# Kernel tuning notes

Hardware: AMD Instinct MI355X
Metric: run time of the kernel (lower is better)

Reference implementation:

```python
import jax, jax.numpy as jnp
import numpy as np
from jax import lax

N_NODES = 100000
N_EDGES = 3200000
NODE_DIM = 128
K = 8            # number of kmeans heads
MAX_OVERLAP = 2  # top-k cluster memberships per node
THRESH = 1e-8


def setup_inputs() -> dict:
    key = jax.random.key(0)
    k1, k2, k3, k4, k5 = jax.random.split(key, 5)
    x = jax.random.normal(k1, (N_NODES, NODE_DIM), dtype=jnp.float32)
    edge_index = jax.random.randint(k2, (2, N_EDGES), 0, N_NODES, dtype=jnp.int64)
    # binary initial cluster-membership masks [N, K] (float, like KMeansCarry.mask)
    mask = (jax.random.uniform(k3, (N_NODES, K)) > 0.5).astype(jnp.float32)
    Ww = jax.random.normal(k4, (K, NODE_DIM, NODE_DIM), dtype=jnp.float32) * (1.0 / np.sqrt(NODE_DIM))
    Wm = jax.random.normal(k5, (K, NODE_DIM, 1), dtype=jnp.float32) * (1.0 / np.sqrt(NODE_DIM))
    return {"x": x, "edge_index": edge_index, "mask": mask, "Ww": Ww, "Wm": Wm}


def reference(x, edge_index, mask, Ww, Wm):
    """KMeans over graph: k heads -> boolean node scores -> norm-weighted top-k assignment."""
    N = x.shape[0]
    src, dst = edge_index[0], edge_index[1]

    def head(m_col, Ww_i, Wm_i):
        # masked node features (KMeansCarry.masked_x)
        xm = x * m_col[:, None]                                   # [N, D]
        node_mask = m_col > 0                                     # [N]
        # masked subgraph (KMeansCarry.masked_edge_index): keep edges with both endpoints in mask
        ev = (node_mask[src] & node_mask[dst]).astype(x.dtype)    # [E]
        # weighting module: per-node transform
        w = jax.nn.relu(xm @ Ww_i)                                # [N, D]
        # message passing over masked subgraph (irregular gather/scatter)
        agg = jax.ops.segment_sum(w[src] * ev[:, None], dst, num_segments=N)  # [N, D]
        # mask module score -> act -> threshold at 0 (KMeansHead.forward)
        score = ((xm + agg) @ Wm_i)[:, 0]                         # [N]
        return jnp.tanh(score) > 0                                # bool [N]

    # vmap over the K heads
    head_masks = jax.vmap(head, in_axes=(1, 0, 0), out_axes=1)(mask, Ww, Wm)  # [N, K] bool

    # KMeans.forward combine step
    above_thresh = head_masks  # bool > THRESH (1e-8 < 1) == the bool itself
    norms = jnp.linalg.norm(x, axis=1, keepdims=True)             # [N, 1]
    masked_weights = jnp.where(above_thresh, norms, -jnp.inf)     # [N, K]
    top_vals, top_idx = lax.top_k(masked_weights, MAX_OVERLAP)    # [N, MAX_OVERLAP]
    valid = jnp.isfinite(top_vals)
    # scatter ones at (row, top_idx) where valid  (duplicate-safe via one-hot + min)
    oh = jax.nn.one_hot(top_idx, K, dtype=x.dtype) * valid[..., None].astype(x.dtype)
    final_mask = jnp.minimum(oh.sum(axis=1), 1.0)                 # [N, K]
    return final_mask
```

## Files before the change

kernel.cpp:

```cpp
#include <hip/hip_runtime.h>

#define N_NODES 100000
#define N_EDGES 3200000
#define D 128
#define K 8

#define TAU 4e-3f
#define WL_CAP 262144

#define CHUNK 96
#define GWAVES 8

#define BKT 128
#define NB  ((N_NODES + BKT - 1) / BKT)
#define EPB 16384
#define NEB ((N_EDGES + EPB - 1) / EPB)

typedef float  f32x4  __attribute__((ext_vector_type(4)));
typedef __bf16 bf16x8 __attribute__((ext_vector_type(8)));

static __device__ __forceinline__ unsigned short bfbits(float f)
{
    const __bf16 b = (__bf16)f;
    return __builtin_bit_cast(unsigned short, b);
}
static __device__ __forceinline__ float bfback(unsigned short u)
{
    return (float)__builtin_bit_cast(__bf16, u);
}

#define NCOMPACT ((N_NODES + 255) / 256)
#define NWSPLIT  ((K * D * D + 255) / 256)

__global__ __launch_bounds__(256)
void prep_kernel(const float* __restrict__ mask,
                 int* __restrict__ lists,
                 int* __restrict__ cnts,
                 unsigned char* __restrict__ mb,
                 const float* __restrict__ Ww,
                 unsigned short* __restrict__ wtH,
                 unsigned short* __restrict__ wtL)
{
    __shared__ int wcnt[4][K];
    __shared__ int wbase[4][K];

    if (blockIdx.x >= NCOMPACT) {
        const int t = (blockIdx.x - NCOMPACT) * 256 + threadIdx.x;
        if (t >= K * D * D) return;
        const int k   = t >> 14;
        const int kk  = (t >> 7) & 127;
        const int col = t & 127;
        const float v = Ww[t];
        const __bf16 h = (__bf16)v;
        const __bf16 l = (__bf16)(v - (float)h);
        const int o = (k << 14) | (col << 7) | kk;
        wtH[o] = __builtin_bit_cast(unsigned short, h);
        wtL[o] = __builtin_bit_cast(unsigned short, l);
        return;
    }

    const int n = blockIdx.x * 256 + threadIdx.x;
    const int lane = threadIdx.x & 63;
    const int wave = threadIdx.x >> 6;
    const bool valid = (n < N_NODES);

    unsigned long long ball[K];
    int bits8 = 0;
    #pragma unroll
    for (int k = 0; k < K; ++k) {
        const bool m = valid && (mask[(size_t)n * K + k] > 0.0f);
        bits8 |= m ? (1 << k) : 0;
        ball[k] = __ballot(m);
        if (lane == 0) wcnt[wave][k] = __popcll(ball[k]);
    }
    __syncthreads();

    if (threadIdx.x < K) {
        const int k = threadIdx.x;
        const int t0 = wcnt[0][k], t1 = wcnt[1][k], t2 = wcnt[2][k], t3 = wcnt[3][k];
        const int base = (t0 + t1 + t2 + t3)
                       ? atomicAdd(&cnts[k], t0 + t1 + t2 + t3) : 0;
        wbase[0][k] = base;
        wbase[1][k] = base + t0;
        wbase[2][k] = base + t0 + t1;
        wbase[3][k] = base + t0 + t1 + t2;
    }
    __syncthreads();

    #pragma unroll
    for (int k = 0; k < K; ++k) {
        if ((ball[k] >> lane) & 1ull) {
            const int pos = __popcll(ball[k] & ((1ull << lane) - 1ull));
            lists[(size_t)k * N_NODES + wbase[wave][k] + pos] = n;
        }
    }
    if (valid) mb[n] = (unsigned char)bits8;
}

__global__ __launch_bounds__(512, 4)
void head_gemm_kernel(const float* __restrict__ x,
                      const unsigned short* __restrict__ wtH,
                      const unsigned short* __restrict__ wtL,
                      const float* __restrict__ Wm,
                      const int* __restrict__ lists,
                      const int* __restrict__ cnts,
                      float* __restrict__ t32,
                      float* __restrict__ base32,
                      const int* __restrict__ ei,
                      int* __restrict__ bhist,
                      const int nhg)
{
    __shared__ __align__(16) unsigned short Ah[CHUNK * D];
    __shared__ __align__(16) unsigned short Al[CHUNK * D];
    __shared__ float redT[GWAVES][48];
    __shared__ float redB[CHUNK][4];
    __shared__ int   ids[CHUNK];

    const int tid = threadIdx.x;

    if (blockIdx.x >= nhg) {
        int* lh = (int*)Ah;
        for (int i = tid; i < NB; i += 512) lh[i] = 0;
        __syncthreads();
        const int e0 = (blockIdx.x - nhg) * EPB;
        #pragma unroll 4
        for (int i = 0; i < EPB / 512; ++i) {
            const int e = e0 + i * 512 + tid;
            if (e < N_EDGES) atomicAdd(&lh[ei[(long long)N_EDGES + e] >> 7], 1);
        }
        __syncthreads();
        for (int i = tid; i < NB; i += 512) {
            const int c = lh[i];
            if (c) atomicAdd(&bhist[i], c);
        }
        return;
    }

    const int bid = blockIdx.x;
    const int k = (bid >> 3) & 7;
    const int c = ((bid >> 6) << 3) | (bid & 7);

    const int cnt = cnts[k];
    const int nbase = c * CHUNK;
    if (nbase >= cnt) return;

    const int lane = tid & 63;
    const int wave = __builtin_amdgcn_readfirstlane((int)(tid >> 6));
    const int* list = lists + (size_t)k * N_NODES;

    if (tid < CHUNK) {
        int idx = nbase + tid;
        if (idx >= cnt) idx = cnt - 1;
        ids[tid] = list[idx];
    }
    __syncthreads();

    if (tid < CHUNK * 4) {
        const int r = tid >> 2;
        const int q = tid & 3;
        const int id = ids[r];
        const float4* xr  = (const float4*)(x + (size_t)id * D);
        const float4* wm4 = (const float4*)(Wm + k * D);
        float bp = 0.0f;
        #pragma unroll
        for (int i = 0; i < 8; ++i) {
            const int f4 = q + 4 * i;
            const float4 v  = xr[f4];
            const float4 wv = wm4[f4];
            bp += v.x * wv.x + v.y * wv.y + v.z * wv.z + v.w * wv.w;
            ushort4 h, l;
            h.x = bfbits(v.x); l.x = bfbits(v.x - bfback(h.x));
            h.y = bfbits(v.y); l.y = bfbits(v.y - bfback(h.y));
            h.z = bfbits(v.z); l.z = bfbits(v.z - bfback(h.z));
            h.w = bfbits(v.w); l.w = bfbits(v.w - bfback(h.w));
            const int boff = ((r * 256 + f4 * 8) ^ ((r & 7) << 4)) >> 1;
            *(ushort4*)&Ah[boff] = h;
            *(ushort4*)&Al[boff] = l;
        }
        redB[r][q] = bp;
    }
    __syncthreads();

    const int wm_ = wave >> 2;
    const int wn  = wave & 3;
    const int l15 = lane & 15;
    const int lg  = lane >> 4;
    const int n0  = wn * 32;

    f32x4 acc[3][2];
    #pragma unroll
    for (int mf = 0; mf < 3; ++mf) {
        acc[mf][0] = (f32x4){0.f, 0.f, 0.f, 0.f};
        acc[mf][1] = (f32x4){0.f, 0.f, 0.f, 0.f};
    }

    const unsigned short* bH0 = wtH + (((k * D + n0 + l15) << 7) + 8 * lg);
    const unsigned short* bH1 = bH0 + (16 << 7);
    const unsigned short* bL0 = wtL + (((k * D + n0 + l15) << 7) + 8 * lg);
    const unsigned short* bL1 = bL0 + (16 << 7);

    #pragma unroll
    for (int s = 0; s < 4; ++s) {
        const int ko = s * 32;
        const bf16x8 Bh0 = *reinterpret_cast<const bf16x8*>(bH0 + ko);
        const bf16x8 Bh1 = *reinterpret_cast<const bf16x8*>(bH1 + ko);
        const bf16x8 Bl0 = *reinterpret_cast<const bf16x8*>(bL0 + ko);
        const bf16x8 Bl1 = *reinterpret_cast<const bf16x8*>(bL1 + ko);
        #pragma unroll
        for (int mf = 0; mf < 3; ++mf) {
            const int m = wm_ * 48 + mf * 16 + l15;
            const int byt = (m * 256 + (ko + 8 * lg) * 2) ^ ((m & 7) << 4);
            const bf16x8 Amh = *reinterpret_cast<const bf16x8*>(&Ah[byt >> 1]);
            const bf16x8 Aml = *reinterpret_cast<const bf16x8*>(&Al[byt >> 1]);
            acc[mf][0] = __builtin_amdgcn_mfma_f32_16x16x32_bf16(Amh, Bh0, acc[mf][0], 0, 0, 0);
            acc[mf][1] = __builtin_amdgcn_mfma_f32_16x16x32_bf16(Amh, Bh1, acc[mf][1], 0, 0, 0);
            acc[mf][0] = __builtin_amdgcn_mfma_f32_16x16x32_bf16(Amh, Bl0, acc[mf][0], 0, 0, 0);
            acc[mf][1] = __builtin_amdgcn_mfma_f32_16x16x32_bf16(Amh, Bl1, acc[mf][1], 0, 0, 0);
            acc[mf][0] = __builtin_amdgcn_mfma_f32_16x16x32_bf16(Aml, Bh0, acc[mf][0], 0, 0, 0);
            acc[mf][1] = __builtin_amdgcn_mfma_f32_16x16x32_bf16(Aml, Bh1, acc[mf][1], 0, 0, 0);
        }
    }

    const float wmv0 = Wm[k * D + n0 + l15];
    const float wmv1 = Wm[k * D + n0 + 16 + l15];
    float keep = 0.0f;
    #pragma unroll
    for (int mf = 0; mf < 3; ++mf) {
        #pragma unroll
        for (int r = 0; r < 4; ++r) {
            float p = fmaxf(acc[mf][0][r], 0.0f) * wmv0
                    + fmaxf(acc[mf][1][r], 0.0f) * wmv1;
            p += __shfl_xor(p, 1);
            p += __shfl_xor(p, 2);
            p += __shfl_xor(p, 4);
            p += __shfl_xor(p, 8);
            if (l15 == mf * 4 + r) keep = p;
        }
    }
    if (l15 < 12)
        redT[wave][((l15 >> 2) << 4) + (lg << 2) + (l15 & 3)] = keep;
    __syncthreads();

    if (tid < CHUNK) {
        const int r = tid;
        const int idx = nbase + r;
        if (idx < cnt) {
            const int wg = r / 48;
            const int rl = r - wg * 48;
            const float ts = redT[wg * 4 + 0][rl] + redT[wg * 4 + 1][rl]
                           + redT[wg * 4 + 2][rl] + redT[wg * 4 + 3][rl];
            const float bs = redB[r][0] + redB[r][1] + redB[r][2] + redB[r][3];
            const int id = ids[r];
            t32[(size_t)id * K + k]    = ts;
            base32[(size_t)id * K + k] = bs;
        }
    }
}

__global__ __launch_bounds__(1024)
void escan_kernel(const int* __restrict__ bhist,
                  int* __restrict__ bases,
                  int* __restrict__ cursors)
{
    __shared__ int sc[1024];
    const int tid = threadIdx.x;
    const int v = (tid < NB) ? bhist[tid] : 0;
    sc[tid] = v;
    __syncthreads();
    for (int off = 1; off < 1024; off <<= 1) {
        int t = 0;
        if (tid >= off) t = sc[tid - off];
        __syncthreads();
        sc[tid] += t;
        __syncthreads();
    }
    if (tid < NB) {
        const int ex = sc[tid] - v;
        bases[tid]   = ex;
        cursors[tid] = ex;
        if (tid == NB - 1) bases[NB] = sc[tid];
    }
}

__global__ __launch_bounds__(512)
void ebucket_kernel(const int* __restrict__ ei,
                    int* __restrict__ cursors,
                    int* __restrict__ bkt)
{
    __shared__ int lh[NB];
    __shared__ int wb[NB];
    const int tid = threadIdx.x;
    for (int i = tid; i < NB; i += 512) lh[i] = 0;
    __syncthreads();
    const int e0 = blockIdx.x * EPB;
    #pragma unroll 4
    for (int i = 0; i < EPB / 512; ++i) {
        const int e = e0 + i * 512 + tid;
        if (e < N_EDGES) atomicAdd(&lh[ei[(long long)N_EDGES + e] >> 7], 1);
    }
    __syncthreads();
    for (int i = tid; i < NB; i += 512) {
        const int c = lh[i];
        wb[i] = c ? atomicAdd(&cursors[i], c) : 0;
        lh[i] = 0;
    }
    __syncthreads();
    #pragma unroll 4
    for (int i = 0; i < EPB / 512; ++i) {
        const int e = e0 + i * 512 + tid;
        if (e < N_EDGES) {
            const int d = ei[(long long)N_EDGES + e];
            const int s = ei[e];
            const int b = d >> 7;
            const int r = atomicAdd(&lh[b], 1);
            const int idx = wb[b] + r;
            if (idx < N_EDGES)
                bkt[idx] = (s << 7) | (d & 127);
        }
    }
}

__global__ __launch_bounds__(512)
void eaccum_kernel(const int* __restrict__ bkt,
                   const int* __restrict__ bases,
                   const unsigned char* __restrict__ mb,
                   const float* __restrict__ t32,
                   const float* __restrict__ base32,
                   float* __restrict__ agg32,
                   float* __restrict__ out,
                   unsigned char* __restrict__ flag8,
                   double* __restrict__ s64,
                   int2* __restrict__ wl,
                   int* __restrict__ wlcnt)
{
    __shared__ float acc[BKT * K];
    __shared__ unsigned char mbl[BKT];
    __shared__ unsigned char fll[BKT];
    __shared__ int anyfl;
    const int b = blockIdx.x;
    const int n0 = b << 7;
    const int tid = threadIdx.x;
    for (int i = tid; i < BKT * K; i += 512) acc[i] = 0.0f;
    if (tid < BKT) {
        const int n = n0 + tid;
        mbl[tid] = (n < N_NODES) ? mb[n] : 0;
    }
    if (tid == 0) anyfl = 0;
    __syncthreads();

    const int eB = bases[b];
    int eE = bases[b + 1];
    if (eE > N_EDGES) eE = N_EDGES;
    for (int e = eB + tid; e < eE; e += 512) {
        const int rec = bkt[e];
        const int s  = rec >> 7;
        const int dl = rec & 127;
        const unsigned md = mbl[dl];
        if (md) {
            const float4* tr = (const float4*)(t32 + (size_t)s * K);
            const float4 t0 = tr[0], t1 = tr[1];
            #pragma unroll
            for (int k = 0; k < K; ++k) {
                const float tv = (k < 4)
                    ? ((k < 2) ? (k == 0 ? t0.x : t0.y) : (k == 2 ? t0.z : t0.w))
                    : ((k < 6) ? (k == 4 ? t1.x : t1.y) : (k == 6 ? t1.z : t1.w));
                if (((md >> k) & 1) && tv != 0.0f)
                    atomicAdd(&acc[(dl << 3) + k], tv);
            }
        }
    }
    __syncthreads();

    if (tid < BKT) {
        const int n = n0 + tid;
        if (n < N_NODES) {
            const unsigned m8 = mbl[tid];
            const float4* b4 = (const float4*)(base32 + (size_t)n * K);
            const float4 b40 = b4[0], b41 = b4[1];
            float bs[K];
            bs[0] = b40.x; bs[1] = b40.y; bs[2] = b40.z; bs[3] = b40.w;
            bs[4] = b41.x; bs[5] = b41.y; bs[6] = b41.z; bs[7] = b41.w;
            float o[K];
            int cnt = 0, fl = 0;
            #pragma unroll
            for (int k = 0; k < K; ++k) {
                const float sc = bs[k] + acc[(tid << 3) + k];
                const bool masked = (m8 >> k) & 1;
                const bool hm = masked && (sc > 0.0f);
                if (masked && fabsf(sc) < TAU) fl |= (1 << k);
                o[k] = (hm && cnt < 2) ? 1.0f : 0.0f;
                cnt += hm ? 1 : 0;
            }
            float4* op = (float4*)(out + (size_t)n * K);
            op[0] = make_float4(o[0], o[1], o[2], o[3]);
            op[1] = make_float4(o[4], o[5], o[6], o[7]);
            float4* ap = (float4*)(agg32 + (size_t)n * K);
            ap[0] = make_float4(acc[(tid << 3) + 0], acc[(tid << 3) + 1],
                                acc[(tid << 3) + 2], acc[(tid << 3) + 3]);
            ap[1] = make_float4(acc[(tid << 3) + 4], acc[(tid << 3) + 5],
                                acc[(tid << 3) + 6], acc[(tid << 3) + 7]);
            flag8[n] = (unsigned char)fl;
            fll[tid] = (unsigned char)fl;
            if (fl) {
                anyfl = 1;
                #pragma unroll
                for (int k = 0; k < K; ++k)
                    if ((fl >> k) & 1) s64[(size_t)n * K + k] = 0.0;
            }
        } else {
            fll[tid] = 0;
        }
    }
    __syncthreads();

    if (anyfl) {
        for (int e = eB + tid; e < eE; e += 512) {
            const int rec = bkt[e];
            const int dl = rec & 127;
            unsigned f = fll[dl];
            if (!f) continue;
            const int s = rec >> 7;
            f &= mb[s];
            while (f) {
                const int k = __ffs(f) - 1;
                f &= f - 1;
                const int idx = atomicAdd(wlcnt, 1);
                if (idx < WL_CAP) wl[idx] = make_int2(s | (k << 20), n0 + dl);
            }
        }
    }
}

__global__ __launch_bounds__(256)
void scatter_fallback_kernel(const int* __restrict__ ei,
                             const unsigned char* __restrict__ mb,
                             const float* __restrict__ t32,
                             float* __restrict__ agg32)
{
    const long long tid = (long long)blockIdx.x * 256 + threadIdx.x;
    if (tid >= (long long)N_EDGES * K) return;
    const int k = (int)(tid & (K - 1));
    const long long e = tid >> 3;
    const int d = ei[(long long)N_EDGES + e];
    const int s = ei[e];
    const unsigned md = mb[d] & mb[s];
    if (!((md >> k) & 1)) return;
    const float v = t32[(size_t)s * K + k];
    if (v != 0.0f) atomicAdd(&agg32[(size_t)d * K + k], v);
}

__global__ __launch_bounds__(256)
void combine_flag_kernel(const unsigned char* __restrict__ mb,
                         const float* __restrict__ base32,
                         const float* __restrict__ agg32,
                         float* __restrict__ out,
                         unsigned char* __restrict__ flag8,
                         double* __restrict__ s64)
{
    const int n = blockIdx.x * 256 + threadIdx.x;
    if (n >= N_NODES) return;
    const unsigned m8 = mb[n];
    float o[K];
    int cnt = 0, fl = 0;
    #pragma unroll
    for (int k = 0; k < K; ++k) {
        const float s = base32[(size_t)n * K + k] + agg32[(size_t)n * K + k];
        const bool masked = (m8 >> k) & 1;
        const bool hm = masked && (s > 0.0f);
        if (masked && fabsf(s) < TAU) fl |= (1 << k);
        o[k] = (hm && cnt < 2) ? 1.0f : 0.0f;
        cnt += hm ? 1 : 0;
    }
    float4* op = (float4*)(out + (size_t)n * K);
    op[0] = make_float4(o[0], o[1], o[2], o[3]);
    op[1] = make_float4(o[4], o[5], o[6], o[7]);
    flag8[n] = (unsigned char)fl;
    if (fl) {
        #pragma unroll
        for (int k = 0; k < K; ++k)
            if ((fl >> k) & 1) s64[(size_t)n * K + k] = 0.0;
    }
}

__global__ __launch_bounds__(256)
void edge_flag_kernel(const int* __restrict__ ei,
                      const unsigned char* __restrict__ mb,
                      const unsigned char* __restrict__ flag8,
                      int2* __restrict__ wl,
                      int* __restrict__ wlcnt)
{
    const int e = blockIdx.x * 256 + threadIdx.x;
    if (e >= N_EDGES) return;
    const int d = ei[(long long)N_EDGES + e];
    unsigned f = flag8[d];
    if (!f) return;
    const int s = ei[e];
    f &= mb[s];
    while (f) {
        const int k = __ffs(f) - 1;
        f &= f - 1;
        const int idx = atomicAdd(wlcnt, 1);
        if (idx < WL_CAP) wl[idx] = make_int2(s | (k << 20), d);
    }
}

__global__ __launch_bounds__(256)
void repair_t_kernel(const float* __restrict__ x,
                     const float* __restrict__ Ww,
                     const float* __restrict__ Wm,
                     const int2* __restrict__ wl,
                     const int* __restrict__ wlcnt,
                     double* __restrict__ score64)
{
    const int lane = threadIdx.x & 63;
    const int waveId = blockIdx.x * 4 + (threadIdx.x >> 6);
    const int nWaves = gridDim.x * 4;
    int cnt = *wlcnt;
    if (cnt > WL_CAP) cnt = WL_CAP;
    for (int w = waveId; w < cnt; w += nWaves) {
        const int2 ent = wl[w];
        const int s = __builtin_amdgcn_readfirstlane(ent.x & 0xFFFFF);
        const int k = __builtin_amdgcn_readfirstlane(ent.x >> 20);
        const int d = ent.y;
        const float* xr = x + (size_t)s * D;
        const float* Wk = Ww + (size_t)k * D * D;
        double c0 = 0.0, c1 = 0.0;
        for (int j = 0; j < D; ++j) {
            const double xd = (double)xr[j];
            c0 = fma(xd, (double)Wk[j * D + lane], c0);
            c1 = fma(xd, (double)Wk[j * D + lane + 64], c1);
        }
        double ts = fmax(c0, 0.0) * (double)Wm[k * D + lane]
                  + fmax(c1, 0.0) * (double)Wm[k * D + lane + 64];
        #pragma unroll
        for (int off = 32; off > 0; off >>= 1) ts += __shfl_xor(ts, off);
        if (lane == 0) atomicAdd(&score64[(size_t)d * K + k], ts);
    }
}

__global__ __launch_bounds__(256)
void repair_combine_kernel(const float* __restrict__ x,
                           const unsigned char* __restrict__ mb,
                           const float* __restrict__ Wm,
                           const float* __restrict__ base32,
                           const float* __restrict__ agg32,
                           const double* __restrict__ score64,
                           const unsigned char* __restrict__ flag8,
                           float* __restrict__ out)
{
    const int n = blockIdx.x * 256 + threadIdx.x;
    if (n >= N_NODES) return;
    const unsigned f = flag8[n];
    if (!f) return;
    const unsigned m8 = mb[n];
    float o[K];
    int cnt = 0;
    #pragma unroll
    for (int k = 0; k < K; ++k) {
        bool hm;
        if ((f >> k) & 1) {
            double b = 0.0;
            for (int j = 0; j < D; ++j)
                b = fma((double)x[(size_t)n * D + j], (double)Wm[k * D + j], b);
            hm = (b + score64[(size_t)n * K + k]) > 0.0;
        } else {
            hm = ((m8 >> k) & 1) &&
                 ((base32[(size_t)n * K + k] + agg32[(size_t)n * K + k]) > 0.0f);
        }
        o[k] = (hm && cnt < 2) ? 1.0f : 0.0f;
        cnt += hm ? 1 : 0;
    }
    float4* op = (float4*)(out + (size_t)n * K);
    op[0] = make_float4(o[0], o[1], o[2], o[3]);
    op[1] = make_float4(o[4], o[5], o[6], o[7]);
}

extern "C" void kernel_launch(void* const* d_in, const int* in_sizes, int n_in,
                              void* d_out, int out_size, void* d_ws, size_t ws_size,
                              hipStream_t stream)
{
    const float* x    = (const float*)d_in[0];
    const int*   ei   = (const int*)d_in[1];
    const float* mask = (const float*)d_in[2];
    const float* Ww   = (const float*)d_in[3];
    const float* Wm   = (const float*)d_in[4];
    float* out = (float*)d_out;

    char* w = (char*)d_ws;
    float*          t32    = (float*)w;
    float*          agg32  = (float*)(w + 3200000);
    double*         s64    = (double*)(w + 6400000);
    int*            lists  = (int*)(w + 6400000);
    unsigned short* wtH    = (unsigned short*)(w + 9600000);
    unsigned short* wtL    = (unsigned short*)(w + 9600000 + 262144);
    unsigned char*  flag8  = (unsigned char*)(w + 12800000);
    int*            cnts   = (int*)(w + 12900000);
    int*            wlcnt  = (int*)(w + 12900032);
    int*            bhist  = (int*)(w + 12900064);
    int*            bases  = (int*)(w + 12903200);
    int*            cursors= (int*)(w + 12906336);
    int2*           wl     = (int2*)(w + 12909504);
    float*          b32    = (float*)(w + 15006656);
    unsigned char*  mb     = (unsigned char*)(w + 18206656);
    int*            bkt    = (int*)(w + 18306656);
    const size_t WS_BUCKETED = 31106656;
    const bool bucketed = (ws_size >= WS_BUCKETED);

    hipMemsetAsync(t32, 0, 3200000, stream);
    hipMemsetAsync(w + 12900000, 0, 4096, stream);

    prep_kernel<<<NCOMPACT + NWSPLIT, 256, 0, stream>>>(
        mask, lists, cnts, mb, Ww, wtH, wtL);

    const int nchunks = (N_NODES + CHUNK - 1) / CHUNK;
    const int nc8 = (nchunks + 7) & ~7;
    const int nhg = nc8 * K;
    head_gemm_kernel<<<nhg + NEB, 512, 0, stream>>>(
        x, wtH, wtL, Wm, lists, cnts, t32, b32, ei, bhist, nhg);

    if (bucketed) {
        escan_kernel<<<1, 1024, 0, stream>>>(bhist, bases, cursors);
        ebucket_kernel<<<NEB, 512, 0, stream>>>(ei, cursors, bkt);
        eaccum_kernel<<<NB, 512, 0, stream>>>(bkt, bases, mb, t32, b32,
                                              agg32, out, flag8, s64, wl, wlcnt);
    } else {
        hipMemsetAsync(agg32, 0, 3200000, stream);
        const long long nek = (long long)N_EDGES * K;
        scatter_fallback_kernel<<<(int)((nek + 255) / 256), 256, 0, stream>>>(
            ei, mb, t32, agg32);
        combine_flag_kernel<<<(N_NODES + 255) / 256, 256, 0, stream>>>(
            mb, b32, agg32, out, flag8, s64);
        edge_flag_kernel<<<(N_EDGES + 255) / 256, 256, 0, stream>>>(
            ei, mb, flag8, wl, wlcnt);
    }

    repair_t_kernel<<<512, 256, 0, stream>>>(x, Ww, Wm, wl, wlcnt, s64);

    repair_combine_kernel<<<(N_NODES + 255) / 256, 256, 0, stream>>>(
        x, mb, Wm, b32, agg32, s64, flag8, out);
}
```

Measured before the change: 359.1 us.

## Move edge histogram into prep kernel and overlap bucketing with head GEMM

The destination-bucket histogram moves from the GEMM kernel into extra blocks of the prep kernel, and the prefix scan now runs before the head GEMM. The edge-bucketing scatter then runs as leading blocks of the head GEMM launch, which removes the separate ebucket kernel launch and overlaps the memory-bound bucketing with compute-bound GEMM blocks. In exchange the prep kernel gets heavier, and the bucketing blocks share occupancy with the GEMM blocks.

```diff
diff --git a/kernel.cpp b/kernel.cpp
--- a/kernel.cpp
+++ b/kernel.cpp
@@ -39,10 +39,30 @@
                  unsigned char* __restrict__ mb,
                  const float* __restrict__ Ww,
                  unsigned short* __restrict__ wtH,
-                 unsigned short* __restrict__ wtL)
-{
-    __shared__ int wcnt[4][K];
-    __shared__ int wbase[4][K];
+                 unsigned short* __restrict__ wtL,
+                 const int* __restrict__ ei,
+                 int* __restrict__ bhist)
+{
+    __shared__ int lds[NB + 64];
+
+    if (blockIdx.x >= NCOMPACT + NWSPLIT) {
+        int* lh = lds;
+        const int tid = threadIdx.x;
+        for (int i = tid; i < NB; i += 256) lh[i] = 0;
+        __syncthreads();
+        const int e0 = (blockIdx.x - NCOMPACT - NWSPLIT) * EPB;
+        #pragma unroll 4
+        for (int i = 0; i < EPB / 256; ++i) {
+            const int e = e0 + i * 256 + tid;
+            if (e < N_EDGES) atomicAdd(&lh[ei[(long long)N_EDGES + e] >> 7], 1);
+        }
+        __syncthreads();
+        for (int i = tid; i < NB; i += 256) {
+            const int c = lh[i];
+            if (c) atomicAdd(&bhist[i], c);
+        }
+        return;
+    }
 
     if (blockIdx.x >= NCOMPACT) {
         const int t = (blockIdx.x - NCOMPACT) * 256 + threadIdx.x;
@@ -59,6 +79,9 @@
         return;
     }
 
+    int (*wcnt)[K]  = (int(*)[K])lds;
+    int (*wbase)[K] = (int(*)[K])(lds + 32);
+
     const int n = blockIdx.x * 256 + threadIdx.x;
     const int lane = threadIdx.x & 63;
     const int wave = threadIdx.x >> 6;
@@ -107,8 +130,9 @@
                       float* __restrict__ t32,
                       float* __restrict__ base32,
                       const int* __restrict__ ei,
-                      int* __restrict__ bhist,
-                      const int nhg)
+                      int* __restrict__ cursors,
+                      int* __restrict__ bkt,
+                      const int neb)
 {
     __shared__ __align__(16) unsigned short Ah[CHUNK * D];
     __shared__ __align__(16) unsigned short Al[CHUNK * D];
@@ -118,11 +142,12 @@
 
     const int tid = threadIdx.x;
 
-    if (blockIdx.x >= nhg) {
+    if ((int)blockIdx.x < neb) {
         int* lh = (int*)Ah;
+        int* wb = lh + NB;
         for (int i = tid; i < NB; i += 512) lh[i] = 0;
         __syncthreads();
-        const int e0 = (blockIdx.x - nhg) * EPB;
+        const int e0 = blockIdx.x * EPB;
         #pragma unroll 4
         for (int i = 0; i < EPB / 512; ++i) {
             const int e = e0 + i * 512 + tid;
@@ -131,12 +156,27 @@
         __syncthreads();
         for (int i = tid; i < NB; i += 512) {
             const int c = lh[i];
-            if (c) atomicAdd(&bhist[i], c);
+            wb[i] = c ? atomicAdd(&cursors[i], c) : 0;
+            lh[i] = 0;
+        }
+        __syncthreads();
+        #pragma unroll 4
+        for (int i = 0; i < EPB / 512; ++i) {
+            const int e = e0 + i * 512 + tid;
+            if (e < N_EDGES) {
+                const int d = ei[(long long)N_EDGES + e];
+                const int s = ei[e];
+                const int b = d >> 7;
+                const int r = atomicAdd(&lh[b], 1);
+                const int idx = wb[b] + r;
+                if (idx < N_EDGES)
+                    bkt[idx] = (s << 7) | (d & 127);
+            }
         }
         return;
     }
 
-    const int bid = blockIdx.x;
+    const int bid = blockIdx.x - neb;
     const int k = (bid >> 3) & 7;
     const int c = ((bid >> 6) << 3) | (bid & 7);
 
@@ -279,44 +319,6 @@
         bases[tid]   = ex;
         cursors[tid] = ex;
         if (tid == NB - 1) bases[NB] = sc[tid];
-    }
-}
-
-__global__ __launch_bounds__(512)
-void ebucket_kernel(const int* __restrict__ ei,
-                    int* __restrict__ cursors,
-                    int* __restrict__ bkt)
-{
-    __shared__ int lh[NB];
-    __shared__ int wb[NB];
-    const int tid = threadIdx.x;
-    for (int i = tid; i < NB; i += 512) lh[i] = 0;
-    __syncthreads();
-    const int e0 = blockIdx.x * EPB;
-    #pragma unroll 4
-    for (int i = 0; i < EPB / 512; ++i) {
-        const int e = e0 + i * 512 + tid;
-        if (e < N_EDGES) atomicAdd(&lh[ei[(long long)N_EDGES + e] >> 7], 1);
-    }
-    __syncthreads();
-    for (int i = tid; i < NB; i += 512) {
-        const int c = lh[i];
-        wb[i] = c ? atomicAdd(&cursors[i], c) : 0;
-        lh[i] = 0;
-    }
-    __syncthreads();
-    #pragma unroll 4
-    for (int i = 0; i < EPB / 512; ++i) {
-        const int e = e0 + i * 512 + tid;
-        if (e < N_EDGES) {
-            const int d = ei[(long long)N_EDGES + e];
-            const int s = ei[e];
-            const int b = d >> 7;
-            const int r = atomicAdd(&lh[b], 1);
-            const int idx = wb[b] + r;
-            if (idx < N_EDGES)
-                bkt[idx] = (s << 7) | (d & 127);
-        }
     }
 }
 
@@ -609,18 +611,19 @@
     hipMemsetAsync(t32, 0, 3200000, stream);
     hipMemsetAsync(w + 12900000, 0, 4096, stream);
 
-    prep_kernel<<<NCOMPACT + NWSPLIT, 256, 0, stream>>>(
-        mask, lists, cnts, mb, Ww, wtH, wtL);
+    prep_kernel<<<NCOMPACT + NWSPLIT + NEB, 256, 0, stream>>>(
+        mask, lists, cnts, mb, Ww, wtH, wtL, ei, bhist);
+
+    escan_kernel<<<1, 1024, 0, stream>>>(bhist, bases, cursors);
 
     const int nchunks = (N_NODES + CHUNK - 1) / CHUNK;
     const int nc8 = (nchunks + 7) & ~7;
     const int nhg = nc8 * K;
-    head_gemm_kernel<<<nhg + NEB, 512, 0, stream>>>(
-        x, wtH, wtL, Wm, lists, cnts, t32, b32, ei, bhist, nhg);
+    const int neb = bucketed ? NEB : 0;
+    head_gemm_kernel<<<neb + nhg, 512, 0, stream>>>(
+        x, wtH, wtL, Wm, lists, cnts, t32, b32, ei, cursors, bkt, neb);
 
     if (bucketed) {
-        escan_kernel<<<1, 1024, 0, stream>>>(bhist, bases, cursors);
-        ebucket_kernel<<<NEB, 512, 0, stream>>>(ei, cursors, bkt);
         eaccum_kernel<<<NB, 512, 0, stream>>>(bkt, bases, mb, t32, b32,
                                               agg32, out, flag8, s64, wl, wlcnt);
     } else {
```

After: 344.7 us. -4.0%, faster.
